# Kernel optimization log

Hardware: AMD Instinct MI355X
Metric: run time of the kernel (lower is better)

The kernel has to match this reference:

```python
import jax, jax.numpy as jnp
import numpy as np

N = 1_000_000   # detections
FDIM = 64       # embedding dim
C = 128         # number of clusters (track ids in [0, C))
DELTA_VAR = 0.5
DELTA_DIST = 3.0


def setup_inputs() -> dict:
    key = jax.random.key(0)
    k1, k2 = jax.random.split(key)
    features = jax.random.normal(k1, (N, FDIM), dtype=jnp.float32)
    labels = jax.random.randint(k2, (N, 2), 0, C, dtype=jnp.int32)  # [fr, track_id], all ids >= 0
    return {"features": features, "labels": labels}


def reference(features, labels):
    # All track ids are >= 0 by construction, so the tp_ids filter is a no-op
    # and the dynamic unique-cluster loop becomes a fixed-C segment reduce.
    ids = labels[:, 1]
    ones = jnp.ones((features.shape[0],), dtype=features.dtype)
    counts = jax.ops.segment_sum(ones, ids, num_segments=C)            # (C,)
    sums = jax.ops.segment_sum(features, ids, num_segments=C)         # (C, F)
    means = sums / counts[:, None]                                     # per-cluster mean

    # variance term: per-point distance to its cluster mean, hinged at delta_var
    d = jnp.linalg.norm(features - means[ids], axis=1)                 # (N,)
    per_pt = jnp.square(jax.nn.relu(d - DELTA_VAR))
    per_cluster = jax.ops.segment_sum(per_pt, ids, num_segments=C) / counts
    var_loss = jnp.sum(per_cluster) / C

    # pairwise cluster-distance term over i != j, hinged at delta_dist
    diff = means[:, None, :] - means[None, :, :]                       # (C, C, F)
    sq = jnp.sum(diff * diff, axis=-1)                                 # (C, C)
    eye = jnp.eye(C, dtype=bool)
    pd = jnp.sqrt(jnp.where(eye, 1.0, sq))                             # safe sqrt on diagonal
    dl = jnp.where(eye, 0.0, jnp.square(jax.nn.relu(DELTA_DIST - pd)))
    dist_loss = jnp.sum(dl) / (C * (C - 1))

    return var_loss + dist_loss
```

## Files before the change

kernel.cpp:

```cpp
#include <hip/hip_runtime.h>

#define NPTS 1000000
#define FDIM 64
#define CNUM 128
#define PSTRIDE 8320
#define NB1 512
#define NB3 1024

typedef _Float16 half8 __attribute__((ext_vector_type(8)));
typedef float f32x4 __attribute__((ext_vector_type(4)));

__global__ __launch_bounds__(256, 2) void k1_partials(
    const float* __restrict__ feats, const int* __restrict__ labels,
    float* __restrict__ partials, int nblocks)
{
    __shared__ float lds[FDIM * 132];
    __shared__ float cntw[4][130];
    const int tid = threadIdx.x;
    const int lane = tid & 63;
    const int n15 = lane & 15;
    const int kb = (lane >> 4) * 8;
    const int rowb = (lane >> 4) * 4;
    const int w = tid >> 6;
    const int nwaves = nblocks * 4;
    const int wid = ((blockIdx.x << 8) + tid) >> 6;

    f32x4 acc[8][4];
    f32x4 accc[8];
    #pragma unroll
    for (int ct = 0; ct < 8; ++ct) {
        accc[ct] = (f32x4){0.f, 0.f, 0.f, 0.f};
        #pragma unroll
        for (int nt = 0; nt < 4; ++nt)
            acc[ct][nt] = (f32x4){0.f, 0.f, 0.f, 0.f};
    }
    half8 B1;
    #pragma unroll
    for (int j = 0; j < 8; ++j) B1[j] = (_Float16)1.0f;

    const int ntiles = NPTS / 32;
    for (int t = wid; t < ntiles; t += nwaves) {
        const int p0 = t * 32;
        const float* fp = feats + (size_t)(p0 + kb) * FDIM + n15;
        const int* lp = labels + 2 * (p0 + kb) + 1;
        int vlab[8];
        #pragma unroll
        for (int i = 0; i < 8; ++i) vlab[i] = lp[2 * i];

        half8 B[4];
        #pragma unroll
        for (int nt = 0; nt < 4; ++nt) {
            #pragma unroll
            for (int i = 0; i < 8; ++i)
                B[nt][i] = (_Float16)fp[i * FDIM + nt * 16];
        }
        #pragma unroll
        for (int ct = 0; ct < 8; ++ct) {
            const int cmine = ct * 16 + n15;
            union { unsigned u[4]; half8 h; } ua;
            #pragma unroll
            for (int j = 0; j < 4; ++j)
                ua.u[j] = ((vlab[2 * j] == cmine) ? 0x3C00u : 0u)
                        | ((vlab[2 * j + 1] == cmine) ? 0x3C000000u : 0u);
            #pragma unroll
            for (int nt = 0; nt < 4; ++nt)
                acc[ct][nt] = __builtin_amdgcn_mfma_f32_16x16x32_f16(
                    ua.h, B[nt], acc[ct][nt], 0, 0, 0);
            accc[ct] = __builtin_amdgcn_mfma_f32_16x16x32_f16(
                ua.h, B1, accc[ct], 0, 0, 0);
        }
    }

    if (n15 == 0) {
        #pragma unroll
        for (int ct = 0; ct < 8; ++ct)
            #pragma unroll
            for (int reg = 0; reg < 4; ++reg)
                cntw[w][ct * 16 + rowb + reg] = accc[ct][reg];
    }

    for (int r = 0; r < 4; ++r) {
        const int q = (w + r) & 3;
        #pragma unroll
        for (int c2 = 0; c2 < 2; ++c2) {
            const int ct = 2 * q + c2;
            #pragma unroll
            for (int nt = 0; nt < 4; ++nt) {
                float* a = &lds[(nt * 16 + n15) * 132 + ct * 16 + rowb];
                if (r == 0) {
                    *(f32x4*)a = acc[ct][nt];
                } else {
                    f32x4 old = *(f32x4*)a;
                    *(f32x4*)a = old + acc[ct][nt];
                }
            }
        }
        __syncthreads();
    }

    float* dst = partials + (size_t)blockIdx.x * PSTRIDE;
    for (int i4 = tid; i4 < 2048; i4 += 256) {
        const int f = i4 >> 5, c0 = (i4 & 31) * 4;
        ((float4*)dst)[i4] = *(float4*)&lds[f * 132 + c0];
    }
    if (tid < CNUM)
        dst[8192 + tid] = cntw[0][tid] + cntw[1][tid] + cntw[2][tid] + cntw[3][tid];
}

__global__ __launch_bounds__(256) void k2_reduce(
    const float* __restrict__ partials, int nblocks, float* __restrict__ red,
    float* __restrict__ ppsum, float* __restrict__ dsum, int* __restrict__ counter)
{
    const int tid = threadIdx.x;
    const int tsub = tid & 31, grp = tid >> 5;
    const int t0 = blockIdx.x * 32;
    float s = 0.f;
    #pragma unroll 8
    for (int b = grp; b < nblocks; b += 8)
        s += partials[(size_t)b * PSTRIDE + t0 + tsub];
    __shared__ float lred[8][33];
    lred[grp][tsub] = s;
    __syncthreads();
    if (tid < 32) {
        float tot = 0.f;
        #pragma unroll
        for (int q = 0; q < 8; ++q) tot += lred[q][tid];
        const int t = t0 + tid;
        if (t < 8192) red[(t & 127) * FDIM + (t >> 7)] = tot;
        else red[t] = tot;
    }
    if (blockIdx.x == 0) {
        if (tid >= 128) ppsum[tid - 128] = 0.f;
        if (tid == 64) dsum[0] = 0.f;
        if (tid == 65) counter[0] = 0;
    }
}

__global__ __launch_bounds__(256, 4) void k3_var(
    const float4* __restrict__ feats4, const int* __restrict__ labels,
    const float* __restrict__ red, float* __restrict__ ppsum, int nblocks)
{
    __shared__ float4 mu4[CNUM * 16];
    __shared__ float lpp[CNUM];
    const int tid = threadIdx.x;
    for (int i = tid; i < 2048; i += 256) {
        float4 sv = ((const float4*)red)[i];
        float ci = 1.0f / red[8192 + (i >> 4)];
        mu4[i] = make_float4(sv.x * ci, sv.y * ci, sv.z * ci, sv.w * ci);
    }
    if (tid < CNUM) lpp[tid] = 0.f;
    __syncthreads();

    const int lane = tid & 63;
    const int k = lane & 15, g = lane >> 4;
    const int nwaves = nblocks * 4;
    const int wid = ((blockIdx.x << 8) + tid) >> 6;
    const int ntiles = NPTS / 32;

    int b = wid;
    float4 v[8]; int cc = 0;
    if (b < ntiles) {
        const float4* fp = feats4 + (size_t)b * 512 + lane;
        #pragma unroll
        for (int s = 0; s < 8; ++s) v[s] = fp[s * 64];
        cc = labels[2 * (b * 32 + (lane & 31)) + 1];
    }
    while (b < ntiles) {
        const int bn = b + nwaves;
        float4 vn[8]; int ccn = 0;
        if (bn < ntiles) {
            const float4* fp = feats4 + (size_t)bn * 512 + lane;
            #pragma unroll
            for (int s = 0; s < 8; ++s) vn[s] = fp[s * 64];
            ccn = labels[2 * (bn * 32 + (lane & 31)) + 1];
        }
        #pragma unroll
        for (int s = 0; s < 8; ++s) {
            const int c = __shfl(cc, 4 * s + g);
            float4 m = mu4[c * 16 + k];
            float dx = v[s].x - m.x, dy = v[s].y - m.y,
                  dz = v[s].z - m.z, dw = v[s].w - m.w;
            float sq = dx * dx + dy * dy + dz * dz + dw * dw;
            sq += __shfl_xor(sq, 1); sq += __shfl_xor(sq, 2);
            sq += __shfl_xor(sq, 4); sq += __shfl_xor(sq, 8);
            if (k == 0) {
                const float t = sqrtf(sq) - 0.5f;
                if (t > 0.f) atomicAdd(&lpp[c], t * t);
            }
        }
        b = bn;
        #pragma unroll
        for (int s = 0; s < 8; ++s) v[s] = vn[s];
        cc = ccn;
    }
    __syncthreads();
    if (tid < CNUM) atomicAdd(&ppsum[tid], lpp[tid]);
}

__global__ __launch_bounds__(128) void k45_dist_final(
    const float* __restrict__ red, const float* __restrict__ ppsum,
    float* __restrict__ dsum, int* __restrict__ counter, float* __restrict__ out)
{
    __shared__ float4 mu4[CNUM * 17];
    __shared__ int lastflag;
    __shared__ float sv[2];
    const int tid = threadIdx.x;
    for (int i = tid; i < 2048; i += 128) {
        float4 s4 = ((const float4*)red)[i];
        float ci = 1.0f / red[8192 + (i >> 4)];
        mu4[(i >> 4) * 17 + (i & 15)] =
            make_float4(s4.x * ci, s4.y * ci, s4.z * ci, s4.w * ci);
    }
    __syncthreads();
    const int i = blockIdx.x, j = tid;
    float sq = 0.f;
    #pragma unroll
    for (int q = 0; q < 16; ++q) {
        float4 a = mu4[i * 17 + q], b = mu4[j * 17 + q];
        float dx = a.x - b.x, dy = a.y - b.y, dz = a.z - b.z, dw = a.w - b.w;
        sq += dx * dx + dy * dy + dz * dz + dw * dw;
    }
    float dl = 0.f;
    if (j != i) {
        const float r = 3.0f - sqrtf(sq);
        if (r > 0.f) dl = r * r;
    }
    #pragma unroll
    for (int m = 1; m < 64; m <<= 1) dl += __shfl_xor(dl, m);
    if ((tid & 63) == 0) atomicAdd(dsum, dl);
    __threadfence();
    __syncthreads();
    if (tid == 0) lastflag = (atomicAdd(counter, 1) == (int)gridDim.x - 1);
    __syncthreads();
    if (lastflag) {
        float v = ppsum[tid] / red[8192 + tid];
        #pragma unroll
        for (int m = 1; m < 64; m <<= 1) v += __shfl_xor(v, m);
        if ((tid & 63) == 0) sv[tid >> 6] = v;
    }
    __syncthreads();
    if (lastflag && tid == 0) {
        const float dtot = atomicAdd(dsum, 0.0f);
        out[0] = (sv[0] + sv[1]) / (float)CNUM
               + dtot / (float)(CNUM * (CNUM - 1));
    }
}

extern "C" void kernel_launch(void* const* d_in, const int* in_sizes, int n_in,
                              void* d_out, int out_size, void* d_ws, size_t ws_size,
                              hipStream_t stream) {
    (void)in_sizes; (void)n_in; (void)out_size;
    const float* feats   = (const float*)d_in[0];
    const float4* feats4 = (const float4*)d_in[0];
    const int* labels    = (const int*)d_in[1];
    float* ws            = (float*)d_ws;
    float* out           = (float*)d_out;

    int nb1 = NB1;
    {
        size_t avail = ws_size / sizeof(float);
        size_t fixed = PSTRIDE + 128 + 2;
        if (avail > fixed) {
            size_t cap = (avail - fixed) / PSTRIDE;
            if ((size_t)nb1 > cap) nb1 = (int)cap;
        } else nb1 = 1;
        if (nb1 < 1) nb1 = 1;
    }
    float* partials = ws;
    float* red      = ws + (size_t)nb1 * PSTRIDE;
    float* ppsum    = red + PSTRIDE;
    float* dsum     = ppsum + 128;
    int*   counter  = (int*)(dsum + 1);

    k1_partials<<<nb1, 256, 0, stream>>>(feats, labels, partials, nb1);
    k2_reduce<<<PSTRIDE / 32, 256, 0, stream>>>(partials, nb1, red, ppsum, dsum, counter);
    k3_var<<<NB3, 256, 0, stream>>>(feats4, labels, red, ppsum, NB3);
    k45_dist_final<<<CNUM, 128, 0, stream>>>(red, ppsum, dsum, counter, out);
}
```

Before: 163.5 us.

## Split feature halves across wave pairs, count via LDS atomics, shrink tiles

The partial-sum kernel now has pairs of waves share each 32-point tile, with each wave covering half of the 64 features. This halves the accumulator registers, raises the launch-bounds occupancy hint to 4, and doubles the block count. The MFMA used for per-cluster counts is replaced by LDS atomic increments from one wave per pair, and the cross-wave LDS merge is simplified. The variance kernel processes 16-point tiles with 4 float4 loads per lane instead of 8, which lowers register pressure but leaves less in flight per wave, and the larger block count enlarges the partials array that k2 must reduce.

```diff
diff --git a/kernel.cpp b/kernel.cpp
--- a/kernel.cpp
+++ b/kernel.cpp
@@ -4,55 +4,58 @@
 #define FDIM 64
 #define CNUM 128
 #define PSTRIDE 8320
-#define NB1 512
+#define NB1 1024
 #define NB3 1024
 
 typedef _Float16 half8 __attribute__((ext_vector_type(8)));
 typedef float f32x4 __attribute__((ext_vector_type(4)));
 
-__global__ __launch_bounds__(256, 2) void k1_partials(
+__global__ __launch_bounds__(256, 4) void k1_partials(
     const float* __restrict__ feats, const int* __restrict__ labels,
     float* __restrict__ partials, int nblocks)
 {
     __shared__ float lds[FDIM * 132];
-    __shared__ float cntw[4][130];
-    const int tid = threadIdx.x;
+    __shared__ float cnt[CNUM];
+    const int tid = threadIdx.x;
+    if (tid < CNUM) cnt[tid] = 0.f;
+    __syncthreads();
+
     const int lane = tid & 63;
     const int n15 = lane & 15;
     const int kb = (lane >> 4) * 8;
     const int rowb = (lane >> 4) * 4;
     const int w = tid >> 6;
-    const int nwaves = nblocks * 4;
-    const int wid = ((blockIdx.x << 8) + tid) >> 6;
-
-    f32x4 acc[8][4];
-    f32x4 accc[8];
+    const int fh = w & 1;
+    const int fbase = fh * 32;
+    const int nstreams = nblocks * 2;
+    const int ts = ((blockIdx.x << 2) + w) >> 1;
+
+    f32x4 acc[8][2];
     #pragma unroll
-    for (int ct = 0; ct < 8; ++ct) {
-        accc[ct] = (f32x4){0.f, 0.f, 0.f, 0.f};
-        #pragma unroll
-        for (int nt = 0; nt < 4; ++nt)
+    for (int ct = 0; ct < 8; ++ct)
+        #pragma unroll
+        for (int nt = 0; nt < 2; ++nt)
             acc[ct][nt] = (f32x4){0.f, 0.f, 0.f, 0.f};
-    }
-    half8 B1;
-    #pragma unroll
-    for (int j = 0; j < 8; ++j) B1[j] = (_Float16)1.0f;
 
     const int ntiles = NPTS / 32;
-    for (int t = wid; t < ntiles; t += nwaves) {
+    for (int t = ts; t < ntiles; t += nstreams) {
         const int p0 = t * 32;
-        const float* fp = feats + (size_t)(p0 + kb) * FDIM + n15;
+        const float* fp = feats + (size_t)(p0 + kb) * FDIM + fbase + n15;
         const int* lp = labels + 2 * (p0 + kb) + 1;
         int vlab[8];
         #pragma unroll
         for (int i = 0; i < 8; ++i) vlab[i] = lp[2 * i];
 
-        half8 B[4];
-        #pragma unroll
-        for (int nt = 0; nt < 4; ++nt) {
+        half8 B[2];
+        #pragma unroll
+        for (int nt = 0; nt < 2; ++nt) {
             #pragma unroll
             for (int i = 0; i < 8; ++i)
                 B[nt][i] = (_Float16)fp[i * FDIM + nt * 16];
+        }
+        if (fh == 0 && lane < 32) {
+            const int myl = labels[2 * (p0 + lane) + 1];
+            atomicAdd(&cnt[myl], 1.0f);
         }
         #pragma unroll
         for (int ct = 0; ct < 8; ++ct) {
@@ -63,37 +66,23 @@
                 ua.u[j] = ((vlab[2 * j] == cmine) ? 0x3C00u : 0u)
                         | ((vlab[2 * j + 1] == cmine) ? 0x3C000000u : 0u);
             #pragma unroll
-            for (int nt = 0; nt < 4; ++nt)
+            for (int nt = 0; nt < 2; ++nt)
                 acc[ct][nt] = __builtin_amdgcn_mfma_f32_16x16x32_f16(
                     ua.h, B[nt], acc[ct][nt], 0, 0, 0);
-            accc[ct] = __builtin_amdgcn_mfma_f32_16x16x32_f16(
-                ua.h, B1, accc[ct], 0, 0, 0);
-        }
-    }
-
-    if (n15 == 0) {
-        #pragma unroll
-        for (int ct = 0; ct < 8; ++ct)
-            #pragma unroll
-            for (int reg = 0; reg < 4; ++reg)
-                cntw[w][ct * 16 + rowb + reg] = accc[ct][reg];
-    }
-
-    for (int r = 0; r < 4; ++r) {
-        const int q = (w + r) & 3;
-        #pragma unroll
-        for (int c2 = 0; c2 < 2; ++c2) {
-            const int ct = 2 * q + c2;
-            #pragma unroll
-            for (int nt = 0; nt < 4; ++nt) {
-                float* a = &lds[(nt * 16 + n15) * 132 + ct * 16 + rowb];
-                if (r == 0) {
-                    *(f32x4*)a = acc[ct][nt];
-                } else {
-                    f32x4 old = *(f32x4*)a;
-                    *(f32x4*)a = old + acc[ct][nt];
+        }
+    }
+    __syncthreads();
+
+    for (int r = 0; r < 2; ++r) {
+        if ((w >> 1) == r) {
+            #pragma unroll
+            for (int ct = 0; ct < 8; ++ct)
+                #pragma unroll
+                for (int nt = 0; nt < 2; ++nt) {
+                    float* a = &lds[(fbase + nt * 16 + n15) * 132 + ct * 16 + rowb];
+                    if (r == 0) *(f32x4*)a = acc[ct][nt];
+                    else        *(f32x4*)a = *(f32x4*)a + acc[ct][nt];
                 }
-            }
         }
         __syncthreads();
     }
@@ -103,8 +92,7 @@
         const int f = i4 >> 5, c0 = (i4 & 31) * 4;
         ((float4*)dst)[i4] = *(float4*)&lds[f * 132 + c0];
     }
-    if (tid < CNUM)
-        dst[8192 + tid] = cntw[0][tid] + cntw[1][tid] + cntw[2][tid] + cntw[3][tid];
+    if (tid < CNUM) dst[8192 + tid] = cnt[tid];
 }
 
 __global__ __launch_bounds__(256) void k2_reduce(
@@ -155,27 +143,27 @@
     const int k = lane & 15, g = lane >> 4;
     const int nwaves = nblocks * 4;
     const int wid = ((blockIdx.x << 8) + tid) >> 6;
-    const int ntiles = NPTS / 32;
+    const int ntiles = NPTS / 16;
 
     int b = wid;
-    float4 v[8]; int cc = 0;
+    float4 v[4]; int cc = 0;
     if (b < ntiles) {
-        const float4* fp = feats4 + (size_t)b * 512 + lane;
-        #pragma unroll
-        for (int s = 0; s < 8; ++s) v[s] = fp[s * 64];
-        cc = labels[2 * (b * 32 + (lane & 31)) + 1];
+        const float4* fp = feats4 + (size_t)b * 256 + lane;
+        #pragma unroll
+        for (int s = 0; s < 4; ++s) v[s] = fp[s * 64];
+        cc = labels[2 * (b * 16 + k) + 1];
     }
     while (b < ntiles) {
         const int bn = b + nwaves;
-        float4 vn[8]; int ccn = 0;
+        float4 vn[4]; int ccn = 0;
         if (bn < ntiles) {
-            const float4* fp = feats4 + (size_t)bn * 512 + lane;
-            #pragma unroll
-            for (int s = 0; s < 8; ++s) vn[s] = fp[s * 64];
-            ccn = labels[2 * (bn * 32 + (lane & 31)) + 1];
-        }
-        #pragma unroll
-        for (int s = 0; s < 8; ++s) {
+            const float4* fp = feats4 + (size_t)bn * 256 + lane;
+            #pragma unroll
+            for (int s = 0; s < 4; ++s) vn[s] = fp[s * 64];
+            ccn = labels[2 * (bn * 16 + k) + 1];
+        }
+        #pragma unroll
+        for (int s = 0; s < 4; ++s) {
             const int c = __shfl(cc, 4 * s + g);
             float4 m = mu4[c * 16 + k];
             float dx = v[s].x - m.x, dy = v[s].y - m.y,
@@ -190,7 +178,7 @@
         }
         b = bn;
         #pragma unroll
-        for (int s = 0; s < 8; ++s) v[s] = vn[s];
+        for (int s = 0; s < 4; ++s) v[s] = vn[s];
         cc = ccn;
     }
     __syncthreads();
```

Result: faster. 132.9 us (-18.7%).
